# Optimization experiments

Measured on AMD Instinct MI355X. Metric: run time of the kernel, lower is better.

## Reference

```python
import jax, jax.numpy as jnp
import numpy as np

NUM_STATES = 8
HIDDEN_DIM = 1024
BATCH = 16384
DT = 0.01
PLANCK = 1.0
EPS_NORM = 1e-8
EPS_LOG = 1e-12


def setup_inputs() -> dict:
    key = jax.random.key(0)
    k1, k2, k3, k4, k5 = jax.random.split(key, 5)
    inv_sqrt_d = 1.0 / np.sqrt(HIDDEN_DIM)
    return {
        "input_state": jax.random.normal(k1, (BATCH, HIDDEN_DIM), dtype=jnp.float32),
        "amplitude_real": jax.random.normal(k2, (NUM_STATES, HIDDEN_DIM), dtype=jnp.float32) * inv_sqrt_d,
        "amplitude_imag": jax.random.normal(k3, (NUM_STATES, HIDDEN_DIM), dtype=jnp.float32) * inv_sqrt_d,
        "hamiltonian": jax.random.normal(k4, (NUM_STATES, NUM_STATES), dtype=jnp.float32) * 0.01,
        "projections": jax.random.normal(k5, (NUM_STATES, HIDDEN_DIM, HIDDEN_DIM), dtype=jnp.float32) * 0.01,
    }


def reference(input_state, amplitude_real, amplitude_imag, hamiltonian, projections):
    # complex amplitudes, normalized per state over hidden dim
    amps = amplitude_real + 1j * amplitude_imag  # [S, D] complex64
    norms = jnp.sum(jnp.abs(amps) ** 2, axis=1, keepdims=True)
    amps = amps / jnp.sqrt(norms + EPS_NORM)

    # unitary Hamiltonian evolution: expm(-i H dt / hbar) on the tiny SxS matrix
    H = (hamiltonian + hamiltonian.T) * 0.5
    U = jax.scipy.linalg.expm((-1j * DT / PLANCK) * H.astype(jnp.complex64))  # [S, S]
    amps = U @ amps  # [S, D]

    # decoherence at time_step=0: factor exp(0)=1, thermal noise scale 0 -> identity

    # superposed output: out[b,e] = sum_s Re(amps[s,e]) * (x @ P_s)[b,e]
    w = jnp.real(amps)  # [S, D]
    proj = jnp.einsum('bd,sde->bse', input_state, projections)  # [B, S, D]
    measured_output = jnp.einsum('bse,se->be', proj, w)  # [B, D]

    # measurement probabilities (computational basis)
    probs = jnp.abs(amps) ** 2
    probs = probs / (probs.sum(axis=0, keepdims=True) + EPS_NORM)
    collapse_prob = probs.mean(axis=1)  # [S]

    # metrics on rank-1 density matrix rho = outer(v, conj(v)), v = amps.flatten():
    # eigenvalues are {||v||^2, 0, ...} so the von Neumann entropy reduces to one term,
    # and sum|rho| = (sum|v|)^2, tr|diag| = sum|v|^2.
    v_abs = jnp.abs(amps.reshape(-1))
    lam = jnp.sum(v_abs ** 2)
    entanglement_entropy = -(lam * jnp.log(lam + EPS_LOG))
    coherence = jnp.sum(v_abs) ** 2 - lam

    amplitude_distribution = jnp.abs(amps) ** 2
    phase_evolution = jnp.angle(amps)

    return (measured_output, collapse_prob, entanglement_entropy, coherence,
            amplitude_distribution, phase_evolution)
```

## Files before the change

### kernel.cpp

```cpp
#include <hip/hip_runtime.h>
#include <hip/hip_bf16.h>

#define NSTATES 8
#define HD      1024
#define NBATCH  16384
#define NT      16

#define OUT_MEAS 0
#define OUT_CP   16777216
#define OUT_ENT  16777224
#define OUT_COH  16777225
#define OUT_AD   16777226
#define OUT_PH   16785418

typedef __attribute__((ext_vector_type(8))) short short8;
typedef __attribute__((ext_vector_type(4))) float f32x4;

__device__ __forceinline__ short f2bf(float f) {
    union { float f; unsigned u; } x; x.f = f;
    unsigned r = x.u + 0x7fffu + ((x.u >> 16) & 1u);
    return (short)(r >> 16);
}

__device__ __forceinline__ unsigned cvtpk(float lo, float hi) {
    unsigned r;
    asm("v_cvt_pk_bf16_f32 %0, %1, %2" : "=v"(r) : "v"(lo), "v"(hi));
    return r;
}

__device__ __forceinline__ short8 pack8pk(float4 a, float4 b) {
    union { unsigned u[4]; short8 s; } r;
    r.u[0] = cvtpk(a.x, a.y);
    r.u[1] = cvtpk(a.z, a.w);
    r.u[2] = cvtpk(b.x, b.y);
    r.u[3] = cvtpk(b.z, b.w);
    return r.s;
}

__global__ __launch_bounds__(1024) void k_amps(const float* __restrict__ AR,
                                               const float* __restrict__ AI,
                                               const float* __restrict__ H,
                                               float* __restrict__ out,
                                               float* __restrict__ w) {
    __shared__ float redA[16 * NSTATES];
    __shared__ float redB[16 * 10];
    __shared__ float norms[NSTATES];
    __shared__ float sA[8][8], sA2[8][8], sA3[8][8];
    __shared__ float Ur[8][8], Ui[8][8];
    __shared__ float lamsa[2];

    const int tid = threadIdx.x;
    const int lane = tid & 63, wid = tid >> 6;
    const int d = tid;

    float arv[NSTATES], aiv[NSTATES];
    #pragma unroll
    for (int s = 0; s < NSTATES; s++) {
        arv[s] = AR[s * HD + d];
        aiv[s] = AI[s * HD + d];
    }
    float p[NSTATES];
    #pragma unroll
    for (int s = 0; s < NSTATES; s++) p[s] = arv[s] * arv[s] + aiv[s] * aiv[s];
    #pragma unroll
    for (int s = 0; s < NSTATES; s++)
        #pragma unroll
        for (int o = 32; o > 0; o >>= 1) p[s] += __shfl_down(p[s], o, 64);
    if (lane == 0)
        #pragma unroll
        for (int s = 0; s < NSTATES; s++) redA[wid * NSTATES + s] = p[s];
    if (tid < 64) {
        int i = tid >> 3, j = tid & 7;
        sA[i][j] = 0.5f * (H[i * 8 + j] + H[j * 8 + i]) * 0.01f;
    }
    __syncthreads();
    if (tid < 8) {
        float acc = 0.f;
        #pragma unroll
        for (int v = 0; v < 16; v++) acc += redA[v * NSTATES + tid];
        norms[tid] = acc;
    }
    if (tid < 64) {
        int i = tid >> 3, j = tid & 7;
        float acc = 0.f;
        #pragma unroll
        for (int k = 0; k < 8; k++) acc += sA[i][k] * sA[k][j];
        sA2[i][j] = acc;
    }
    __syncthreads();
    if (tid < 64) {
        int i = tid >> 3, j = tid & 7;
        float acc = 0.f;
        #pragma unroll
        for (int k = 0; k < 8; k++) acc += sA2[i][k] * sA[k][j];
        sA3[i][j] = acc;
        Ur[i][j] = ((i == j) ? 1.f : 0.f) - 0.5f * sA2[i][j];
        Ui[i][j] = -(sA[i][j] - sA3[i][j] * (1.f / 6.f));
    }
    __syncthreads();

    #pragma unroll
    for (int s = 0; s < NSTATES; s++) {
        float inv = 1.0f / sqrtf(norms[s] + 1e-8f);
        arv[s] *= inv;
        aiv[s] *= inv;
    }
    float nr[NSTATES], ni[NSTATES];
    #pragma unroll
    for (int s = 0; s < NSTATES; s++) {
        float xr = 0.f, xi = 0.f;
        #pragma unroll
        for (int t = 0; t < NSTATES; t++) {
            float ur = Ur[s][t], ui = Ui[s][t];
            xr += ur * arv[t] - ui * aiv[t];
            xi += ur * aiv[t] + ui * arv[t];
        }
        nr[s] = xr; ni[s] = xi;
    }
    float dist[NSTATES], csum = 0.f, sabs = 0.f;
    #pragma unroll
    for (int s = 0; s < NSTATES; s++) {
        dist[s] = nr[s] * nr[s] + ni[s] * ni[s];
        csum += dist[s];
        sabs += sqrtf(dist[s]);
    }
    #pragma unroll
    for (int s = 0; s < NSTATES; s++) {
        out[OUT_AD + s * HD + d] = dist[s];
        out[OUT_PH + s * HD + d] = atan2f(ni[s], nr[s]);
        w[s * HD + d] = nr[s];
    }
    float cinv = 1.0f / (csum + 1e-8f);
    float q[10];
    #pragma unroll
    for (int s = 0; s < NSTATES; s++) q[s] = dist[s] * cinv;
    q[8] = csum; q[9] = sabs;
    #pragma unroll
    for (int v = 0; v < 10; v++)
        #pragma unroll
        for (int o = 32; o > 0; o >>= 1) q[v] += __shfl_down(q[v], o, 64);
    if (lane == 0)
        #pragma unroll
        for (int v = 0; v < 10; v++) redB[wid * 10 + v] = q[v];
    __syncthreads();
    if (tid < 10) {
        float acc = 0.f;
        #pragma unroll
        for (int v = 0; v < 16; v++) acc += redB[v * 10 + tid];
        if (tid < 8)       out[OUT_CP + tid] = acc * (1.0f / HD);
        else               lamsa[tid - 8] = acc;
    }
    __syncthreads();
    if (tid == 0) {
        float lam = lamsa[0], sa = lamsa[1];
        out[OUT_ENT] = -(lam * logf(lam + 1e-12f));
        out[OUT_COH] = sa * sa - lam;
    }
}

__global__ __launch_bounds__(256) void k_project_t(const float* __restrict__ P,
                                                   const float* __restrict__ w,
                                                   short* __restrict__ Mt) {
    __shared__ float tile[64][65];
    int d0 = (blockIdx.x >> 4) * 64;
    int e0 = (blockIdx.x & 15) * 64;
    int tx = threadIdx.x & 63, ty = threadIdx.x >> 6;
    float wv[NSTATES];
    #pragma unroll
    for (int s = 0; s < NSTATES; s++) wv[s] = w[s * HD + e0 + tx];
    #pragma unroll
    for (int j = 0; j < 16; j++) {
        int r = ty + 4 * j;
        float acc = 0.f;
        #pragma unroll
        for (int s = 0; s < NSTATES; s++)
            acc += wv[s] * P[(size_t)s * HD * HD + (size_t)(d0 + r) * HD + e0 + tx];
        tile[r][tx] = acc;
    }
    __syncthreads();
    #pragma unroll
    for (int j = 0; j < 16; j++) {
        int er = ty + 4 * j;
        Mt[(size_t)(e0 + er) * HD + d0 + tx] = f2bf(tile[tx][er]);
    }
}


__device__ __forceinline__ void stage_half_B(const short* __restrict__ srcBase,
                                             int rowbase, int h, int t2,
                                             short* dst, const int* goff,
                                             const int* ldsoff) {
    #pragma unroll
    for (int i = 0; i < 2; i++) {
        const short* g = srcBase + (size_t)(rowbase + h * 128) * HD + t2 * 64 + goff[i];
        __builtin_amdgcn_global_load_lds(
            (const __attribute__((address_space(1))) void*)g,
            (__attribute__((address_space(3))) void*)(dst + h * 8192 + ldsoff[i]),
            16, 0, 0);
    }
}

#define XLOAD(dst, h, t2)                                                      \
    {                                                                          \
        const float* b_ = X + (size_t)(brow + (h) * 128) * HD + (t2) * 64;     \
        dst[0] = *reinterpret_cast<const float4*>(b_ + goff[0]);               \
        dst[1] = *reinterpret_cast<const float4*>(b_ + goff[0] + 4);           \
        dst[2] = *reinterpret_cast<const float4*>(b_ + goff[1]);               \
        dst[3] = *reinterpret_cast<const float4*>(b_ + goff[1] + 4);           \
    }

#define XWRITE(dstlds, src)                                                    \
    {                                                                          \
        *reinterpret_cast<short8*>((dstlds) + ldsoff[0]) = pack8pk(src[0], src[1]); \
        *reinterpret_cast<short8*>((dstlds) + ldsoff[1]) = pack8pk(src[2], src[3]); \
    }

#define LOAD_A(qa)                                                             \
    _Pragma("unroll") for (int mf = 0; mf < 4; mf++)                           \
    _Pragma("unroll") for (int kk = 0; kk < 2; kk++)                           \
        af[mf][kk] = *reinterpret_cast<const short8*>(                         \
            &Acur[((qa) * 128 + wr64 + mf * 16 + ln15) * 64 + kx[kk]]);

#define LOAD_B_TO(dst, qb)                                                     \
    _Pragma("unroll") for (int nf = 0; nf < 2; nf++)                           \
    _Pragma("unroll") for (int kk = 0; kk < 2; kk++)                           \
        dst[nf][kk] = *reinterpret_cast<const short8*>(                        \
            &Bcur[((qb) * 128 + wn32 + nf * 16 + ln15) * 64 + kx[kk]]);

#define MFMA_P(qa, qb, breg)                                                   \
    _Pragma("unroll") for (int mf = 0; mf < 4; mf++)                           \
    _Pragma("unroll") for (int nf = 0; nf < 2; nf++)                           \
    _Pragma("unroll") for (int kk = 0; kk < 2; kk++)                           \
        acc[(qa) * 4 + mf][(qb) * 2 + nf] =                                    \
            __builtin_amdgcn_mfma_f32_16x16x32_bf16(                           \
                af[mf][kk], breg[nf][kk], acc[(qa) * 4 + mf][(qb) * 2 + nf], 0, 0, 0);

__global__ __launch_bounds__(512, 1) void k_gemm_jit(const float* __restrict__ X,
                                                     const short* __restrict__ Mt,
                                                     float* __restrict__ out) {
    __shared__ short As[2][256 * 64];
    __shared__ short Bs[2][256 * 64];

    const int bid = blockIdx.x;
    const int swz = (bid & 7) * 32 + (bid >> 3);
    const int brow = (swz >> 2) * 256;
    const int bcol = (swz & 3) * 256;

    const int tid  = threadIdx.x;
    const int lane = tid & 63, wid = tid >> 6;
    const int wr = wid >> 2, wn = wid & 3;
    const int ln15 = lane & 15, l16 = lane >> 4;
    const int wr64 = wr * 64;
    const int wn32 = wn * 32;

    int kx[2];
    kx[0] = ((l16 + 0) ^ (ln15 & 7)) * 8;
    kx[1] = ((l16 + 4) ^ (ln15 & 7)) * 8;

    int goff[2], ldsoff[2];
    #pragma unroll
    for (int i = 0; i < 2; i++) {
        int c = tid + 512 * i;
        int row = c >> 3, kc = c & 7;
        goff[i]   = row * HD + ((kc ^ (row & 7)) * 8);
        ldsoff[i] = c * 8;
    }

    short* A0 = &As[0][0]; short* A1b = &As[1][0];
    short* B0 = &Bs[0][0]; short* B1b = &Bs[1][0];

    f32x4 acc[8][4];
    #pragma unroll
    for (int m = 0; m < 8; m++)
        #pragma unroll
        for (int n = 0; n < 4; n++) acc[m][n] = (f32x4){0.f, 0.f, 0.f, 0.f};

    float4 xrL[4], xrH[4];

    XLOAD(xrL, 0, 0);
    XLOAD(xrH, 1, 0);
    stage_half_B(Mt, bcol, 0, 0, B0, goff, ldsoff);
    stage_half_B(Mt, bcol, 1, 0, B0, goff, ldsoff);
    stage_half_B(Mt, bcol, 1, 1, B1b, goff, ldsoff);
    XWRITE(A0, xrL);
    XWRITE(A0 + 8192, xrH);
    asm volatile("s_waitcnt vmcnt(2) lgkmcnt(0)" ::: "memory");
    __builtin_amdgcn_s_barrier();

    short8 af[4][2], bfL[2][2], bfH[2][2];

    #pragma unroll 1
    for (int t = 0; t < NT; t++) {
        const int cur = t & 1;
        short* Acur  = cur ? A1b : A0;
        short* Bcur  = cur ? B1b : B0;
        short* Anext = cur ? A0 : A1b;
        short* Bnext = cur ? B0 : B1b;

        LOAD_A(0); LOAD_B_TO(bfL, 0);
        if (t + 1 < NT) XLOAD(xrL, 0, (t + 1));
        __builtin_amdgcn_s_barrier();
        __builtin_amdgcn_s_setprio(1);
        MFMA_P(0, 0, bfL);
        __builtin_amdgcn_s_setprio(0);

        LOAD_B_TO(bfH, 1);
        if (t + 1 < NT) {
            XLOAD(xrH, 1, (t + 1));
            stage_half_B(Mt, bcol, 0, t + 1, Bnext, goff, ldsoff);
        }
        __builtin_amdgcn_s_barrier();
        __builtin_amdgcn_s_setprio(1);
        MFMA_P(0, 1, bfH);
        __builtin_amdgcn_s_setprio(0);

        LOAD_A(1);
        if (t + 1 < NT) XWRITE(Anext, xrL);
        __builtin_amdgcn_s_barrier();
        __builtin_amdgcn_s_setprio(1);
        MFMA_P(1, 1, bfH);
        __builtin_amdgcn_s_setprio(0);

        if (t + 1 < NT) XWRITE(Anext + 8192, xrH);
        if (t + 2 < NT) stage_half_B(Mt, bcol, 1, t + 2, Bcur, goff, ldsoff);
        if (t + 2 < NT)      asm volatile("s_waitcnt vmcnt(2) lgkmcnt(0)" ::: "memory");
        else if (t + 1 < NT) asm volatile("s_waitcnt vmcnt(0) lgkmcnt(0)" ::: "memory");
        __builtin_amdgcn_s_barrier();
        __builtin_amdgcn_s_setprio(1);
        MFMA_P(1, 0, bfL);
        __builtin_amdgcn_s_setprio(0);
    }

    #pragma unroll
    for (int qa = 0; qa < 2; qa++)
        #pragma unroll
        for (int mf = 0; mf < 4; mf++)
            #pragma unroll
            for (int qb = 0; qb < 2; qb++)
                #pragma unroll
                for (int nf = 0; nf < 2; nf++)
                    #pragma unroll
                    for (int j = 0; j < 4; j++) {
                        int r = brow + qa * 128 + wr64 + mf * 16 + l16 * 4 + j;
                        int c = bcol + qb * 128 + wn32 + nf * 16 + ln15;
                        out[(size_t)r * HD + c] = acc[qa * 4 + mf][qb * 2 + nf][j];
                    }
}

extern "C" void kernel_launch(void* const* d_in, const int* in_sizes, int n_in,
                              void* d_out, int out_size, void* d_ws, size_t ws_size,
                              hipStream_t stream) {
    const float* X  = (const float*)d_in[0];
    const float* AR = (const float*)d_in[1];
    const float* AI = (const float*)d_in[2];
    const float* H  = (const float*)d_in[3];
    const float* P  = (const float*)d_in[4];
    float* out = (float*)d_out;

    char* ws = (char*)d_ws;
    float* w  = (float*)ws;
    short* Mt = (short*)(ws + 32768);

    k_amps<<<1, 1024, 0, stream>>>(AR, AI, H, out, w);
    k_project_t<<<256, 256, 0, stream>>>(P, w, Mt);
    k_gemm_jit<<<(NBATCH / 256) * (HD / 256), 512, 0, stream>>>(X, Mt, out);
}
```

Baseline: 72.08 us.

## Deepen X prefetch to two tiles ahead with double register buffers

The GEMM main loop now prefetches the fp32 input tile two iterations ahead into alternating register buffers, unrolling the loop by two so the buffers swap statically. B staging for the next tile is moved earlier, and the vmcnt waits are relaxed so more global loads stay in flight. This hides more global-load latency for the activation tile, at the cost of extra VGPRs (32 more floats per thread) under a 1-wave-per-SIMD launch bound, and depends on the hand-counted vmcnt values being correct.

```diff
diff --git a/kernel.cpp b/kernel.cpp
--- a/kernel.cpp
+++ b/kernel.cpp
@@ -235,9 +235,51 @@
             __builtin_amdgcn_mfma_f32_16x16x32_bf16(                           \
                 af[mf][kk], breg[nf][kk], acc[(qa) * 4 + mf][(qb) * 2 + nf], 0, 0, 0);
 
-__global__ __launch_bounds__(512, 1) void k_gemm_jit(const float* __restrict__ X,
-                                                     const short* __restrict__ Mt,
-                                                     float* __restrict__ out) {
+#define TILE_BODY(t, WIL, WIH, WWL, WWH)                                       \
+    {                                                                          \
+        const int cur = (t) & 1;                                               \
+        short* Acur  = cur ? A1b : A0;                                         \
+        short* Bcur  = cur ? B1b : B0;                                         \
+        short* Anext = cur ? A0 : A1b;                                         \
+        short* Bnext = cur ? B0 : B1b;                                         \
+                           \
+        LOAD_A(0); LOAD_B_TO(bfL, 0);                                          \
+        if ((t) + 1 < NT) stage_half_B(Mt, bcol, 0, (t) + 1, Bnext, goff, ldsoff); \
+        if ((t) + 2 < NT) XLOAD(WIL, 0, (t) + 2);                              \
+        __builtin_amdgcn_s_barrier();                                          \
+        __builtin_amdgcn_s_setprio(1);                                         \
+        MFMA_P(0, 0, bfL);                                                     \
+        __builtin_amdgcn_s_setprio(0);                                         \
+                                          \
+        LOAD_B_TO(bfH, 1);                                                     \
+        if ((t) + 2 < NT) XLOAD(WIH, 1, (t) + 2);                              \
+        __builtin_amdgcn_s_barrier();                                          \
+        __builtin_amdgcn_s_setprio(1);                                         \
+        MFMA_P(0, 1, bfH);                                                     \
+        __builtin_amdgcn_s_setprio(0);                                         \
+           \
+        LOAD_A(1);                                                             \
+        if ((t) + 1 < NT) XWRITE(Anext, WWL);                                  \
+        __builtin_amdgcn_s_barrier();                                          \
+        __builtin_amdgcn_s_setprio(1);                                         \
+        MFMA_P(1, 1, bfH);                                                     \
+        __builtin_amdgcn_s_setprio(0);                                         \
+            \
+        if ((t) + 1 < NT) XWRITE(Anext + 8192, WWH);                           \
+        if ((t) + 2 < NT) stage_half_B(Mt, bcol, 1, (t) + 2, Bcur, goff, ldsoff); \
+         \
+        \
+        if ((t) + 2 < NT)      asm volatile("s_waitcnt vmcnt(10) lgkmcnt(0)" ::: "memory"); \
+        else if ((t) + 1 < NT) asm volatile("s_waitcnt vmcnt(0) lgkmcnt(0)" ::: "memory");  \
+        __builtin_amdgcn_s_barrier();                                          \
+        __builtin_amdgcn_s_setprio(1);                                         \
+        MFMA_P(1, 0, bfL);                                                     \
+        __builtin_amdgcn_s_setprio(0);                                         \
+    }
+
+__global__ __launch_bounds__(512, 1) void k_gemm_jit2(const float* __restrict__ X,
+                                                      const short* __restrict__ Mt,
+                                                      float* __restrict__ out) {
     __shared__ short As[2][256 * 64];
     __shared__ short Bs[2][256 * 64];
 
@@ -275,60 +317,26 @@
         #pragma unroll
         for (int n = 0; n < 4; n++) acc[m][n] = (f32x4){0.f, 0.f, 0.f, 0.f};
 
-    float4 xrL[4], xrH[4];
-
-    XLOAD(xrL, 0, 0);
-    XLOAD(xrH, 1, 0);
+    float4 W0L[4], W0H[4], W1L[4], W1H[4];
+
+    XLOAD(W0L, 0, 0);
+    XLOAD(W0H, 1, 0);
     stage_half_B(Mt, bcol, 0, 0, B0, goff, ldsoff);
     stage_half_B(Mt, bcol, 1, 0, B0, goff, ldsoff);
     stage_half_B(Mt, bcol, 1, 1, B1b, goff, ldsoff);
-    XWRITE(A0, xrL);
-    XWRITE(A0 + 8192, xrH);
-    asm volatile("s_waitcnt vmcnt(2) lgkmcnt(0)" ::: "memory");
+    XWRITE(A0, W0L);
+    XWRITE(A0 + 8192, W0H);
+    XLOAD(W1L, 0, 1);
+    XLOAD(W1H, 1, 1);
+    asm volatile("s_waitcnt vmcnt(10) lgkmcnt(0)" ::: "memory");
     __builtin_amdgcn_s_barrier();
 
     short8 af[4][2], bfL[2][2], bfH[2][2];
 
     #pragma unroll 1
-    for (int t = 0; t < NT; t++) {
-        const int cur = t & 1;
-        short* Acur  = cur ? A1b : A0;
-        short* Bcur  = cur ? B1b : B0;
-        short* Anext = cur ? A0 : A1b;
-        short* Bnext = cur ? B0 : B1b;
-
-        LOAD_A(0); LOAD_B_TO(bfL, 0);
-        if (t + 1 < NT) XLOAD(xrL, 0, (t + 1));
-        __builtin_amdgcn_s_barrier();
-        __builtin_amdgcn_s_setprio(1);
-        MFMA_P(0, 0, bfL);
-        __builtin_amdgcn_s_setprio(0);
-
-        LOAD_B_TO(bfH, 1);
-        if (t + 1 < NT) {
-            XLOAD(xrH, 1, (t + 1));
-            stage_half_B(Mt, bcol, 0, t + 1, Bnext, goff, ldsoff);
-        }
-        __builtin_amdgcn_s_barrier();
-        __builtin_amdgcn_s_setprio(1);
-        MFMA_P(0, 1, bfH);
-        __builtin_amdgcn_s_setprio(0);
-
-        LOAD_A(1);
-        if (t + 1 < NT) XWRITE(Anext, xrL);
-        __builtin_amdgcn_s_barrier();
-        __builtin_amdgcn_s_setprio(1);
-        MFMA_P(1, 1, bfH);
-        __builtin_amdgcn_s_setprio(0);
-
-        if (t + 1 < NT) XWRITE(Anext + 8192, xrH);
-        if (t + 2 < NT) stage_half_B(Mt, bcol, 1, t + 2, Bcur, goff, ldsoff);
-        if (t + 2 < NT)      asm volatile("s_waitcnt vmcnt(2) lgkmcnt(0)" ::: "memory");
-        else if (t + 1 < NT) asm volatile("s_waitcnt vmcnt(0) lgkmcnt(0)" ::: "memory");
-        __builtin_amdgcn_s_barrier();
-        __builtin_amdgcn_s_setprio(1);
-        MFMA_P(1, 0, bfL);
-        __builtin_amdgcn_s_setprio(0);
+    for (int tt = 0; tt < NT; tt += 2) {
+        TILE_BODY(tt,     W0L, W0H, W1L, W1H);
+        TILE_BODY(tt + 1, W1L, W1H, W0L, W0H);
     }
 
     #pragma unroll
@@ -363,5 +371,5 @@
 
     k_amps<<<1, 1024, 0, stream>>>(AR, AI, H, out, w);
     k_project_t<<<256, 256, 0, stream>>>(P, w, Mt);
-    k_gemm_jit<<<(NBATCH / 256) * (HD / 256), 512, 0, stream>>>(X, Mt, out);
-}
+    k_gemm_jit2<<<(NBATCH / 256) * (HD / 256), 512, 0, stream>>>(X, Mt, out);
+}
```

New measurement: 93.64 us. 29.9% more time.
